# Optimization experiments

Measured on AMD Instinct MI355X. Metric: run time of the kernel, lower is better.

## Reference

```python
import jax, jax.numpy as jnp
import numpy as np

NUM_ITER = 3
HEADS = 8
EPS = 1e-8

def _ln(x, g, b, eps=1e-5):
    mu = x.mean(-1, keepdims=True)
    var = ((x - mu) ** 2).mean(-1, keepdims=True)
    return (x - mu) * jax.lax.rsqrt(var + eps) * g + b

def setup_inputs() -> dict:
    key = jax.random.key(0)
    ks = jax.random.split(key, 10)
    B, Nkv, Din = 32, 4096, 256
    Nq, S, Hm = 16, 256, 512
    def xav(k, shape):
        lim = (6.0 / (shape[0] + shape[1])) ** 0.5
        return jax.random.uniform(k, shape, minval=-lim, maxval=lim, dtype=jnp.float32)
    return {
        "slots": jax.random.normal(ks[0], (Nq, S), dtype=jnp.float32),
        "inputs": jax.random.normal(ks[1], (B, Nkv, Din), dtype=jnp.float32),
        "norm_in_g": jnp.ones((Din,), jnp.float32), "norm_in_b": jnp.zeros((Din,), jnp.float32),
        "norm_slots_g": jnp.ones((S,), jnp.float32), "norm_slots_b": jnp.zeros((S,), jnp.float32),
        "norm_mlp_g": jnp.ones((S,), jnp.float32), "norm_mlp_b": jnp.zeros((S,), jnp.float32),
        "Wq": xav(ks[2], (S, S)), "Wk": xav(ks[3], (S, Din)), "Wv": xav(ks[4], (S, Din)),
        "gru_wih": xav(ks[5], (3 * S, S)),
        "gru_whh": jax.random.normal(ks[6], (3 * S, S), dtype=jnp.float32) * (1.0 / S ** 0.5),
        "gru_bih": jnp.zeros((3 * S,), jnp.float32), "gru_bhh": jnp.zeros((3 * S,), jnp.float32),
        "mlp_w1": xav(ks[7], (Hm, S)), "mlp_b1": jnp.zeros((Hm,), jnp.float32),
        "mlp_w2": xav(ks[8], (S, Hm)), "mlp_b2": jnp.zeros((S,), jnp.float32),
    }

def reference(slots, inputs, norm_in_g, norm_in_b, norm_slots_g, norm_slots_b,
              norm_mlp_g, norm_mlp_b, Wq, Wk, Wv, gru_wih, gru_whh, gru_bih, gru_bhh,
              mlp_w1, mlp_b1, mlp_w2, mlp_b2):
    B, Nkv, Din = inputs.shape
    Nq, S = slots.shape
    H = HEADS
    hd = S // H
    slots = jnp.broadcast_to(slots, (B, Nq, S))
    x = _ln(inputs, norm_in_g, norm_in_b)
    k = (x @ Wk.T).reshape(B, Nkv, H, hd).transpose(0, 2, 1, 3) * (hd ** -0.5)  # [B,H,Nkv,hd]
    v = (x @ Wv.T).reshape(B, Nkv, H, hd).transpose(0, 2, 1, 3)
    attn_vis = None
    for _ in range(NUM_ITER):
        slots_prev = slots
        s = _ln(slots, norm_slots_g, norm_slots_b)
        q = (s @ Wq.T).reshape(B, Nq, H, hd).transpose(0, 2, 1, 3)  # [B,H,Nq,hd]
        # logits [B,Nkv,H*Nq]; softmax jointly over heads and slots per key (slot-axis softmax)
        logits = jnp.einsum('bhkd,bhqd->bkhq', k, q).reshape(B, Nkv, H * Nq)
        attn = jax.nn.softmax(logits, axis=-1).reshape(B, Nkv, H, Nq).transpose(0, 2, 1, 3)  # [B,H,Nkv,Nq]
        attn_vis = attn.sum(1)  # [B,Nkv,Nq]
        attn_n = attn / (attn.sum(axis=2, keepdims=True) + EPS)  # normalize over keys
        updates = jnp.einsum('bhkq,bhkd->bqhd', attn_n, v).reshape(B, Nq, S)
        # GRUCell: gates order r,z,n
        xg = updates.reshape(-1, S)
        h = slots_prev.reshape(-1, S)
        gi = xg @ gru_wih.T + gru_bih
        gh = h @ gru_whh.T + gru_bhh
        ir, iz, inn = jnp.split(gi, 3, axis=-1)
        hr, hz, hn = jnp.split(gh, 3, axis=-1)
        r = jax.nn.sigmoid(ir + hr)
        z = jax.nn.sigmoid(iz + hz)
        n = jnp.tanh(inn + r * hn)
        slots = ((1.0 - z) * n + z * h).reshape(B, Nq, S)
        m = _ln(slots, norm_mlp_g, norm_mlp_b)
        slots = slots + (jax.nn.relu(m @ mlp_w1.T + mlp_b1) @ mlp_w2.T + mlp_b2)
    return (slots, attn_vis)
```

## Files before the change

kernel.cpp:

```cpp
#include <hip/hip_runtime.h>
#include <stdint.h>

typedef unsigned short u16;
typedef __attribute__((ext_vector_type(8))) _Float16 half8;
typedef __attribute__((ext_vector_type(4))) _Float16 half4;
typedef __attribute__((ext_vector_type(4))) float floatx4;

__device__ inline float bflo(unsigned u){ return __uint_as_float(u << 16); }
__device__ inline float bfhi(unsigned u){ return __uint_as_float(u & 0xffff0000u); }
__device__ inline float bf1(u16 v){ return __uint_as_float(((unsigned)v) << 16); }
__device__ inline u16 f2bf(float f){
  unsigned u = __float_as_uint(f);
  u += 0x7fffu + ((u >> 16) & 1u);
  return (u16)(u >> 16);
}
__device__ inline float dot8(uint4 w, float4 a, float4 b, float acc){
  acc = fmaf(bflo(w.x), a.x, acc); acc = fmaf(bfhi(w.x), a.y, acc);
  acc = fmaf(bflo(w.y), a.z, acc); acc = fmaf(bfhi(w.y), a.w, acc);
  acc = fmaf(bflo(w.z), b.x, acc); acc = fmaf(bfhi(w.z), b.y, acc);
  acc = fmaf(bflo(w.w), b.z, acc); acc = fmaf(bfhi(w.w), b.w, acc);
  return acc;
}

#define CW_SLOTS 0
#define CW_GIN   4096
#define CW_BIN   4352
#define CW_GS    4608
#define CW_BS    4864
#define CW_GM    5120
#define CW_BM    5376
#define CW_WQ    5632
#define CW_WK    71168
#define CW_WV    136704
#define CW_WIH   202240
#define CW_WHH   398848
#define CW_BIH   595456
#define CW_BHH   596224
#define CW_W1    596992
#define CW_B1    728064
#define CW_W2    728576
#define CW_B2    859648
#define CW_TOTAL 859904

__global__ void k_flag(const u16* __restrict__ probe, int* __restrict__ flag){
  int t = threadIdx.x;
  int bad = 0;
  #pragma unroll
  for (int i = 0; i < 4; i++){
    float x = bf1(probe[t + i * 256]);
    if (!(fabsf(x) < 1e6f)) bad = 1;
  }
  __shared__ int s;
  if (t == 0) s = 0;
  __syncthreads();
  if (bad) atomicOr(&s, 1);
  __syncthreads();
  if (t == 0) *flag = s;
}

struct CanonArgs { const void* p[18]; };

__global__ void k_canon(CanonArgs a, const int* __restrict__ flag, u16* __restrict__ cw){
  const int off[19] = {CW_SLOTS, CW_GIN, CW_BIN, CW_GS, CW_BS, CW_GM, CW_BM, CW_WQ,
                       CW_WK, CW_WV, CW_WIH, CW_WHH, CW_BIH, CW_BHH, CW_W1, CW_B1,
                       CW_W2, CW_B2, CW_TOTAL};
  int i = blockIdx.x * 256 + threadIdx.x;
  if (i >= CW_TOTAL) return;
  int f32m = *flag;
  int j = 0;
  while (i >= off[j + 1]) j++;
  int local = i - off[j];
  float v = f32m ? ((const float*)a.p[j])[local] : bf1(((const u16*)a.p[j])[local]);
  cw[i] = f2bf(v);
}

__global__ void k_init(const u16* __restrict__ cw, float* __restrict__ slots,
                       _Float16* __restrict__ wkvh)
{
  int idx = blockIdx.x * 256 + threadIdx.x;
  if (idx < 131072){
    float g = bf1(cw[CW_GIN + (idx & 255)]);
    wkvh[idx] = (_Float16)(bf1(cw[CW_WK + idx]) * g);
  } else {
    int i = idx - 131072;
    int d = i & 255;
    int q = (i >> 8) & 15;
    slots[i] = bf1(cw[CW_SLOTS + q * 256 + d]);
  }
}

__global__ void k_beta(const u16* __restrict__ cw, float* __restrict__ beta){
  int c = blockIdx.x * 256 + threadIdx.x;
  if (c >= 512) return;
  float a = 0.f;
  for (int d = 0; d < 256; d++)
    a = fmaf(bf1(cw[CW_BIN + d]), bf1(cw[CW_WK + c * 256 + d]), a);
  beta[c] = a;
}

__global__ void k_zero(float* __restrict__ p, int n){
  int i = blockIdx.x * 256 + threadIdx.x;
  if (i < n) p[i] = 0.f;
}

__global__ __launch_bounds__(256) void k0_stats(
    const void* __restrict__ inp, const int* __restrict__ flag, float2* __restrict__ stats)
{
  int f32m = *flag;
  int g = blockIdx.x * 256 + threadIdx.x;
  int row = g >> 4, l = g & 15;
  float sum = 0.f, sq = 0.f;
  if (f32m){
    const float* rp = (const float*)inp + row * 256 + l * 16;
    #pragma unroll
    for (int i = 0; i < 4; i++){
      float4 v = ((const float4*)rp)[i];
      sum += v.x + v.y + v.z + v.w;
      sq = fmaf(v.x, v.x, sq); sq = fmaf(v.y, v.y, sq);
      sq = fmaf(v.z, v.z, sq); sq = fmaf(v.w, v.w, sq);
    }
  } else {
    const u16* rp = (const u16*)inp + row * 256 + l * 16;
    #pragma unroll
    for (int i = 0; i < 2; i++){
      uint4 u = ((const uint4*)rp)[i];
      unsigned w[4] = {u.x, u.y, u.z, u.w};
      #pragma unroll
      for (int p = 0; p < 4; p++){
        float a = bflo(w[p]), b = bfhi(w[p]);
        sum += a + b; sq = fmaf(a, a, sq); sq = fmaf(b, b, sq);
      }
    }
  }
  #pragma unroll
  for (int m = 1; m < 16; m <<= 1){ sum += __shfl_xor(sum, m); sq += __shfl_xor(sq, m); }
  if (l == 0){
    float mu = sum * (1.f/256.f);
    float var = sq * (1.f/256.f) - mu * mu;
    stats[row] = make_float2(mu, rsqrtf(var + 1e-5f));
  }
}

__global__ __launch_bounds__(256) void k1_gemm(
    const void* __restrict__ inp, const int* __restrict__ flag,
    const float2* __restrict__ stats, const float* __restrict__ beta,
    const _Float16* __restrict__ wkvh, _Float16* __restrict__ kh, _Float16* __restrict__ vT)
{
  int f32m = *flag;
  int tid = threadIdx.x;
  int wv = tid >> 6, lane = tid & 63;
  int m16 = lane & 15, q4 = lane >> 4;
  int nb = blockIdx.y;
  long rowb0 = (long)blockIdx.x * 128;
  int colW = nb * 256 + wv * 64;

  half8 bfr[4][8];
  #pragma unroll
  for (int nt = 0; nt < 4; nt++)
    #pragma unroll
    for (int s = 0; s < 8; s++)
      bfr[nt][s] = *(const half8*)(wkvh + (colW + nt * 16 + m16) * 256 + s * 32 + q4 * 8);

  float bet[4];
  #pragma unroll
  for (int nt = 0; nt < 4; nt++) bet[nt] = beta[colW + nt * 16 + m16];

  for (int rt = 0; rt < 8; rt++){
    long rowb = rowb0 + rt * 16;
    long myRow = rowb + m16;
    float2 st = stats[myRow];
    float mu = st.x, rstd = st.y;

    half8 af[8];
    if (f32m){
      const float* rp = (const float*)inp + myRow * 256 + q4 * 8;
      #pragma unroll
      for (int s = 0; s < 8; s++){
        float4 x0 = *(const float4*)(rp + s * 32);
        float4 x1 = *(const float4*)(rp + s * 32 + 4);
        af[s][0] = (_Float16)((x0.x - mu) * rstd); af[s][1] = (_Float16)((x0.y - mu) * rstd);
        af[s][2] = (_Float16)((x0.z - mu) * rstd); af[s][3] = (_Float16)((x0.w - mu) * rstd);
        af[s][4] = (_Float16)((x1.x - mu) * rstd); af[s][5] = (_Float16)((x1.y - mu) * rstd);
        af[s][6] = (_Float16)((x1.z - mu) * rstd); af[s][7] = (_Float16)((x1.w - mu) * rstd);
      }
    } else {
      const u16* rp = (const u16*)inp + myRow * 256 + q4 * 8;
      #pragma unroll
      for (int s = 0; s < 8; s++){
        uint4 xu = *(const uint4*)(rp + s * 32);
        unsigned xw[4] = {xu.x, xu.y, xu.z, xu.w};
        #pragma unroll
        for (int p = 0; p < 4; p++){
          af[s][2*p]   = (_Float16)((bflo(xw[p]) - mu) * rstd);
          af[s][2*p+1] = (_Float16)((bfhi(xw[p]) - mu) * rstd);
        }
      }
    }

    floatx4 acc[4];
    #pragma unroll
    for (int nt = 0; nt < 4; nt++){
      acc[nt][0] = bet[nt]; acc[nt][1] = bet[nt]; acc[nt][2] = bet[nt]; acc[nt][3] = bet[nt];
    }
    #pragma unroll
    for (int s = 0; s < 8; s++)
      #pragma unroll
      for (int nt = 0; nt < 4; nt++)
        acc[nt] = __builtin_amdgcn_mfma_f32_16x16x32_f16(af[s], bfr[nt][s], acc[nt], 0, 0, 0);

    if (nb == 0){
      long crow = rowb + q4 * 4;
      #pragma unroll
      for (int nt = 0; nt < 4; nt++)
        #pragma unroll
        for (int r = 0; r < 4; r++)
          kh[(crow + r) * 256 + colW + nt * 16 + m16] = (_Float16)acc[nt][r];
    } else {
      int b = (int)(rowb >> 12);
      int key = ((int)rowb & 4095) + q4 * 4;
      #pragma unroll
      for (int nt = 0; nt < 4; nt++){
        int cv = (colW - 256) + nt * 16 + m16;
        half4 pk;
        pk[0] = (_Float16)acc[nt][0]; pk[1] = (_Float16)acc[nt][1];
        pk[2] = (_Float16)acc[nt][2]; pk[3] = (_Float16)acc[nt][3];
        *(half4*)(vT + ((long)b * 256 + cv) * 4096 + key) = pk;
      }
    }
  }
}

__global__ __launch_bounds__(256) void k2_q(
    const float* __restrict__ slots, const u16* __restrict__ cw, _Float16* __restrict__ qh)
{
  const u16* gq = cw + CW_GS;
  const u16* bq = cw + CW_BS;
  const u16* Wq = cw + CW_WQ;
  int row = blockIdx.x, tid = threadIdx.x;
  int wv = tid >> 6, lane = tid & 63;
  float x = slots[row * 256 + tid];
  float s = x, s2 = x * x;
  #pragma unroll
  for (int m = 1; m < 64; m <<= 1){ s += __shfl_xor(s, m); s2 += __shfl_xor(s2, m); }
  __shared__ float red[8];
  if (lane == 0){ red[wv] = s; red[4 + wv] = s2; }
  __syncthreads();
  float tot  = red[0] + red[1] + red[2] + red[3];
  float tot2 = red[4] + red[5] + red[6] + red[7];
  float mu = tot * (1.f/256.f);
  float rstd = rsqrtf(tot2 * (1.f/256.f) - mu * mu + 1e-5f);
  __shared__ float sln[256];
  sln[tid] = (x - mu) * rstd * bf1(gq[tid]) + bf1(bq[tid]);
  __syncthreads();
  const u16* wr = Wq + tid * 256;
  float a = 0.f;
  for (int k = 0; k < 256; k += 8){
    uint4 wu = *(const uint4*)(wr + k);
    float4 l0 = *(const float4*)(sln + k);
    float4 l1 = *(const float4*)(sln + k + 4);
    a = dot8(wu, l0, l1, a);
  }
  qh[row * 256 + tid] = (_Float16)(a * 0.17677669529663687f);
}

__global__ __launch_bounds__(256) void k3_attn(
    const _Float16* __restrict__ kh, const _Float16* __restrict__ vT,
    const _Float16* __restrict__ qh,
    float* __restrict__ denom, float* __restrict__ numer,
    void* __restrict__ out_scratch, const int* __restrict__ flag, int lastIter)
{
  int f32m = *flag;
  int tid = threadIdx.x;
  int wv = tid >> 6, lane = tid & 63;
  int m16 = lane & 15, q4 = lane >> 4;
  int b = blockIdx.x, chunk = blockIdx.y;
  __shared__ float lds_l[32 * 129];

  half8 qf[2];
  #pragma unroll
  for (int hh = 0; hh < 2; hh++){
    int h = wv * 2 + hh;
    qf[hh] = *(const half8*)(qh + (b * 16 + m16) * 256 + h * 32 + q4 * 8);
  }
  float pd[2] = {0.f, 0.f};
  floatx4 un[2][2];
  #pragma unroll
  for (int hh = 0; hh < 2; hh++)
    #pragma unroll
    for (int dt = 0; dt < 2; dt++) un[hh][dt] = (floatx4)0.f;

  half8 afp[2][2];
  {
    int key0 = chunk * 256;
    #pragma unroll
    for (int sub = 0; sub < 2; sub++){
      long rowb = (long)b * 4096 + key0 + sub * 16;
      #pragma unroll
      for (int hh = 0; hh < 2; hh++)
        afp[sub][hh] = *(const half8*)(kh + (rowb + m16) * 256 + (wv * 2 + hh) * 32 + q4 * 8);
    }
  }

  floatx4 z4 = (floatx4)0.f;
  for (int g4 = 0; g4 < 8; g4++){
    int key0 = chunk * 256 + g4 * 32;
    #pragma unroll
    for (int sub = 0; sub < 2; sub++){
      #pragma unroll
      for (int hh = 0; hh < 2; hh++){
        int h = wv * 2 + hh;
        floatx4 d = __builtin_amdgcn_mfma_f32_16x16x32_f16(afp[sub][hh], qf[hh], z4, 0, 0, 0);
        #pragma unroll
        for (int r = 0; r < 4; r++)
          lds_l[(sub * 16 + q4 * 4 + r) * 129 + h * 16 + m16] = d[r];
      }
    }
    if (g4 < 7){
      int keyn = key0 + 32;
      #pragma unroll
      for (int sub = 0; sub < 2; sub++){
        long rowb = (long)b * 4096 + keyn + sub * 16;
        #pragma unroll
        for (int hh = 0; hh < 2; hh++)
          afp[sub][hh] = *(const half8*)(kh + (rowb + m16) * 256 + (wv * 2 + hh) * 32 + q4 * 8);
      }
    }
    __syncthreads();
    half8 vfr[2][2];
    #pragma unroll
    for (int hh = 0; hh < 2; hh++)
      #pragma unroll
      for (int dt = 0; dt < 2; dt++)
        vfr[hh][dt] = *(const half8*)(vT + ((long)b * 256 + (wv * 2 + hh) * 32 + dt * 16 + m16) * 4096 + key0 + q4 * 8);
    {
      int qq = tid & 15;
      #pragma unroll
      for (int half_ = 0; half_ < 2; half_++){
        int kk = (tid >> 4) + half_ * 16;
        float l[8];
        #pragma unroll
        for (int h8 = 0; h8 < 8; h8++) l[h8] = lds_l[kk * 129 + h8 * 16 + qq];
        float M = l[0];
        #pragma unroll
        for (int h8 = 1; h8 < 8; h8++) M = fmaxf(M, l[h8]);
        #pragma unroll
        for (int msk = 1; msk < 16; msk <<= 1) M = fmaxf(M, __shfl_xor(M, msk));
        float p[8], sl = 0.f;
        #pragma unroll
        for (int h8 = 0; h8 < 8; h8++){ p[h8] = __expf(l[h8] - M); sl += p[h8]; }
        float St = sl;
        #pragma unroll
        for (int msk = 1; msk < 16; msk <<= 1) St += __shfl_xor(St, msk);
        float rS = 1.f / St;
        if (lastIter){
          float av = sl * rS;
          long idx = 131072 + ((long)b * 4096 + key0 + kk) * 16 + qq;
          if (f32m) ((float*)out_scratch)[idx] = av;
          else      ((u16*)out_scratch)[idx]   = f2bf(av);
        }
        #pragma unroll
        for (int h8 = 0; h8 < 8; h8++) lds_l[kk * 129 + h8 * 16 + qq] = p[h8] * rS;
      }
    }
    __syncthreads();
    #pragma unroll
    for (int hh = 0; hh < 2; hh++){
      int h = wv * 2 + hh;
      float pv[8];
      #pragma unroll
      for (int j = 0; j < 8; j++) pv[j] = lds_l[(q4 * 8 + j) * 129 + h * 16 + m16];
      float ps = 0.f;
      #pragma unroll
      for (int j = 0; j < 8; j++) ps += pv[j];
      pd[hh] += ps;
      half8 bfr;
      #pragma unroll
      for (int j = 0; j < 8; j++) bfr[j] = (_Float16)pv[j];
      #pragma unroll
      for (int dt = 0; dt < 2; dt++)
        un[hh][dt] = __builtin_amdgcn_mfma_f32_16x16x32_f16(vfr[hh][dt], bfr, un[hh][dt], 0, 0, 0);
    }
    __syncthreads();
  }
  _Float16* pp = (_Float16*)((u16*)out_scratch + (f32m ? 262144 : 131072))
                 + (long)chunk * 131072;
  #pragma unroll
  for (int hh = 0; hh < 2; hh++){
    int h = wv * 2 + hh;
    float t = pd[hh];
    t += __shfl_xor(t, 16); t += __shfl_xor(t, 32);
    if (q4 == 0) atomicAdd(&denom[(b * 8 + h) * 16 + m16], t);
    if (lastIter){
      #pragma unroll
      for (int dt = 0; dt < 2; dt++)
        #pragma unroll
        for (int r = 0; r < 4; r++)
          atomicAdd(&numer[((b * 8 + h) * 16 + m16) * 32 + dt * 16 + q4 * 4 + r], un[hh][dt][r]);
    } else {
      #pragma unroll
      for (int dt = 0; dt < 2; dt++){
        half4 st;
        #pragma unroll
        for (int r = 0; r < 4; r++) st[r] = (_Float16)un[hh][dt][r];
        *(half4*)(pp + ((b * 8 + h) * 16 + m16) * 32 + dt * 16 + q4 * 4) = st;
      }
    }
  }
}

__global__ void k_reduce(const void* __restrict__ out_scratch, const int* __restrict__ flag,
                         float* __restrict__ numer){
  int i = blockIdx.x * 256 + threadIdx.x;
  int f32m = *flag;
  const _Float16* pp = (const _Float16*)((const u16*)out_scratch + (f32m ? 262144 : 131072));
  float s = 0.f;
  #pragma unroll
  for (int c = 0; c < 16; c++) s += (float)pp[(long)c * 131072 + i];
  numer[i] = s;
}

__global__ __launch_bounds__(256) void k4a_gru(
    const float* __restrict__ slots, const float* __restrict__ numer, const float* __restrict__ denom,
    const u16* __restrict__ cw, float* __restrict__ mid)
{
  const u16* wih = cw + CW_WIH;
  const u16* whh = cw + CW_WHH;
  const u16* bih = cw + CW_BIH;
  const u16* bhh = cw + CW_BHH;
  int jc = blockIdx.x, rg = blockIdx.y;
  int tid = threadIdx.x;
  __shared__ float u_s[8][256];
  __shared__ float h_s[8][256];
  {
    int hh = tid >> 5, dh = tid & 31;
    for (int i = 0; i < 8; i++){
      int row = rg * 8 + i;
      int b = row >> 4, slot = row & 15;
      float den = denom[(b * 8 + hh) * 16 + slot] + 1e-8f;
      u_s[i][tid] = numer[((b * 8 + hh) * 16 + slot) * 32 + dh] / den;
      h_s[i][tid] = slots[row * 256 + tid];
    }
  }
  __syncthreads();
  int rl = tid >> 5, jl = tid & 31;
  int j = jc * 32 + jl;
  int row = rg * 8 + rl;
  const u16* wir = wih + j * 256;
  const u16* wiz = wih + (256 + j) * 256;
  const u16* win = wih + (512 + j) * 256;
  const u16* whr = whh + j * 256;
  const u16* whz = whh + (256 + j) * 256;
  const u16* whn = whh + (512 + j) * 256;
  float air = 0, aiz = 0, ain = 0, ahr = 0, ahz = 0, ahn = 0;
  for (int k = 0; k < 256; k += 8){
    float4 u0 = *(const float4*)(&u_s[rl][k]);
    float4 u1 = *(const float4*)(&u_s[rl][k + 4]);
    float4 h0 = *(const float4*)(&h_s[rl][k]);
    float4 h1 = *(const float4*)(&h_s[rl][k + 4]);
    air = dot8(*(const uint4*)(wir + k), u0, u1, air);
    aiz = dot8(*(const uint4*)(wiz + k), u0, u1, aiz);
    ain = dot8(*(const uint4*)(win + k), u0, u1, ain);
    ahr = dot8(*(const uint4*)(whr + k), h0, h1, ahr);
    ahz = dot8(*(const uint4*)(whz + k), h0, h1, ahz);
    ahn = dot8(*(const uint4*)(whn + k), h0, h1, ahn);
  }
  float gr = air + bf1(bih[j])       + ahr + bf1(bhh[j]);
  float gz = aiz + bf1(bih[256 + j]) + ahz + bf1(bhh[256 + j]);
  float r = 1.f / (1.f + __expf(-gr));
  float z = 1.f / (1.f + __expf(-gz));
  float nn = tanhf(ain + bf1(bih[512 + j]) + r * (ahn + bf1(bhh[512 + j])));
  float h = h_s[rl][j];
  mid[row * 256 + j] = (1.f - z) * nn + z * h;
}

__global__ __launch_bounds__(256) void k4b_mlp(
    const float* __restrict__ mid, const u16* __restrict__ cw,
    float* __restrict__ slots, void* __restrict__ out_base,
    const int* __restrict__ flag, int lastIter)
{
  int f32m = *flag;
  const u16* gm = cw + CW_GM;
  const u16* bm = cw + CW_BM;
  const u16* w1 = cw + CW_W1;
  const u16* b1 = cw + CW_B1;
  const u16* w2 = cw + CW_W2;
  const u16* b2 = cw + CW_B2;
  int row = blockIdx.x, tid = threadIdx.x;
  int wv = tid >> 6, lane = tid & 63;
  float x = mid[row * 256 + tid];
  float s = x, s2 = x * x;
  #pragma unroll
  for (int m = 1; m < 64; m <<= 1){ s += __shfl_xor(s, m); s2 += __shfl_xor(s2, m); }
  __shared__ float red[8];
  if (lane == 0){ red[wv] = s; red[4 + wv] = s2; }
  __syncthreads();
  float tot  = red[0] + red[1] + red[2] + red[3];
  float tot2 = red[4] + red[5] + red[6] + red[7];
  float mu = tot * (1.f/256.f);
  float rstd = rsqrtf(tot2 * (1.f/256.f) - mu * mu + 1e-5f);
  __shared__ float ls[256];
  __shared__ float h1[512];
  ls[tid] = (x - mu) * rstd * bf1(gm[tid]) + bf1(bm[tid]);
  __syncthreads();
  const u16* w1a = w1 + tid * 256;
  const u16* w1b = w1 + (tid + 256) * 256;
  float a0 = 0.f, a1 = 0.f;
  for (int k = 0; k < 256; k += 8){
    float4 l0 = *(const float4*)(ls + k);
    float4 l1 = *(const float4*)(ls + k + 4);
    a0 = dot8(*(const uint4*)(w1a + k), l0, l1, a0);
    a1 = dot8(*(const uint4*)(w1b + k), l0, l1, a1);
  }
  h1[tid]       = fmaxf(a0 + bf1(b1[tid]), 0.f);
  h1[tid + 256] = fmaxf(a1 + bf1(b1[tid + 256]), 0.f);
  __syncthreads();
  const u16* w2r = w2 + tid * 512;
  float a = 0.f;
  for (int k = 0; k < 512; k += 8){
    float4 l0 = *(const float4*)(h1 + k);
    float4 l1 = *(const float4*)(h1 + k + 4);
    a = dot8(*(const uint4*)(w2r + k), l0, l1, a);
  }
  float res = x + a + bf1(b2[tid]);
  slots[row * 256 + tid] = res;
  if (lastIter){
    int idx = row * 256 + tid;
    if (f32m) ((float*)out_base)[idx] = res;
    else      ((u16*)out_base)[idx]   = f2bf(res);
  }
}

extern "C" void kernel_launch(void* const* d_in, const int* in_sizes, int n_in,
                              void* d_out, int out_size, void* d_ws, size_t ws_size,
                              hipStream_t stream)
{
  char* ws = (char*)d_ws;
  int*  flagp    = (int*)ws;
  u16*  cw       = (u16*)(ws + 256);
  _Float16* qh   = (_Float16*)(ws + 1720064);
  _Float16* wkvh = (_Float16*)(ws + 1982208);
  float* slots   = (float*)(ws + 2244352);
  float* mid     = (float*)(ws + 2768640);
  float* numer   = (float*)(ws + 3292928);
  float* denom   = (float*)(ws + 3817216);
  _Float16* kh   = (_Float16*)(ws + 3833600);
  _Float16* vT   = (_Float16*)(ws + 70942464);
  float2* stats  = (float2*)(ws + 2768640);
  float*  beta   = (float*)(ws + 3817216);

  CanonArgs ca;
  ca.p[0]  = d_in[0];   ca.p[1]  = d_in[2];   ca.p[2]  = d_in[3];
  ca.p[3]  = d_in[4];   ca.p[4]  = d_in[5];   ca.p[5]  = d_in[6];
  ca.p[6]  = d_in[7];   ca.p[7]  = d_in[8];   ca.p[8]  = d_in[9];
  ca.p[9]  = d_in[10];  ca.p[10] = d_in[11];  ca.p[11] = d_in[12];
  ca.p[12] = d_in[13];  ca.p[13] = d_in[14];  ca.p[14] = d_in[15];
  ca.p[15] = d_in[16];  ca.p[16] = d_in[17];  ca.p[17] = d_in[18];

  k_flag<<<1, 256, 0, stream>>>((const u16*)d_in[1], flagp);
  k_canon<<<(CW_TOTAL + 255) / 256, 256, 0, stream>>>(ca, flagp, cw);
  k_init<<<1024, 256, 0, stream>>>(cw, slots, wkvh);
  k_beta<<<2, 256, 0, stream>>>(cw, beta);
  k0_stats<<<8192, 256, 0, stream>>>(d_in[1], flagp, stats);
  k1_gemm<<<dim3(1024, 2), 256, 0, stream>>>(d_in[1], flagp, stats, beta, wkvh, kh, vT);
  for (int it = 0; it < 3; it++){
    int last = (it == 2) ? 1 : 0;
    k2_q<<<512, 256, 0, stream>>>(slots, cw, qh);
    if (last) k_zero<<<528, 256, 0, stream>>>(numer, 135168);
    else      k_zero<<<16, 256, 0, stream>>>(denom, 4096);
    k3_attn<<<dim3(32, 16), 256, 0, stream>>>(kh, vT, qh, denom, numer, d_out, flagp, last);
    if (!last) k_reduce<<<512, 256, 0, stream>>>(d_out, flagp, numer);
    k4a_gru<<<dim3(8, 64), 256, 0, stream>>>(slots, numer, denom, cw, mid);
    k4b_mlp<<<512, 256, 0, stream>>>(mid, cw, slots, d_out, flagp, last);
  }
}
```

Measured before the change: 791.4 us.

## Restructure K/V projection GEMM into narrower tiles with software-pipelined input loads

The K/V projection kernel now gives each wave a single 16-column tile instead of four, on a grid of 8 column blocks by 1024 row blocks. The next row tile's input loads are issued before the current tile's MFMAs run, so global load latency overlaps compute. The fp32/bf16 branch becomes a template parameter. In exchange, each input row is read and normalized four times more often, since each block now covers 64 columns rather than 256.

```diff
diff --git a/kernel.cpp b/kernel.cpp
--- a/kernel.cpp
+++ b/kernel.cpp
@@ -141,93 +141,111 @@
   }
 }
 
+template<int F32>
+__device__ __forceinline__ void k1_body(
+    const void* __restrict__ inp, const float2* __restrict__ stats,
+    const float* __restrict__ beta, const _Float16* __restrict__ wkvh,
+    _Float16* __restrict__ kh, _Float16* __restrict__ vT,
+    int nb, long rowb0, int colW, int m16, int q4)
+{
+  half8 bfr[8];
+  #pragma unroll
+  for (int s = 0; s < 8; s++)
+    bfr[s] = *(const half8*)(wkvh + (colW + m16) * 256 + s * 32 + q4 * 8);
+  float bet = beta[colW + m16];
+
+  constexpr int NR = F32 ? 16 : 8;
+  uint4 raw[NR];
+  half8 af[8];
+  float2 stp;
+
+  auto ISSUE = [&](long rowb){
+    long myRow = rowb + m16;
+    stp = stats[myRow];
+    if (F32){
+      const uint4* rp = (const uint4*)((const float*)inp + myRow * 256 + q4 * 8);
+      #pragma unroll
+      for (int s = 0; s < 8; s++){ raw[2*s] = rp[s*8]; raw[2*s+1] = rp[s*8+1]; }
+    } else {
+      const uint4* rp = (const uint4*)((const u16*)inp + myRow * 256 + q4 * 8);
+      #pragma unroll
+      for (int s = 0; s < 8; s++) raw[s] = rp[s*4];
+    }
+  };
+
+  auto CONVERT = [&](){
+    float mu = stp.x, rstd = stp.y;
+    if (F32){
+      #pragma unroll
+      for (int s = 0; s < 8; s++){
+        float x[8] = { __uint_as_float(raw[2*s].x), __uint_as_float(raw[2*s].y),
+                       __uint_as_float(raw[2*s].z), __uint_as_float(raw[2*s].w),
+                       __uint_as_float(raw[2*s+1].x), __uint_as_float(raw[2*s+1].y),
+                       __uint_as_float(raw[2*s+1].z), __uint_as_float(raw[2*s+1].w) };
+        #pragma unroll
+        for (int p = 0; p < 8; p++)
+          af[s][p] = (_Float16)((x[p] - mu) * rstd);
+      }
+    } else {
+      #pragma unroll
+      for (int s = 0; s < 8; s++){
+        unsigned xw[4] = {raw[s].x, raw[s].y, raw[s].z, raw[s].w};
+        #pragma unroll
+        for (int p = 0; p < 4; p++){
+          af[s][2*p]   = (_Float16)((bflo(xw[p]) - mu) * rstd);
+          af[s][2*p+1] = (_Float16)((bfhi(xw[p]) - mu) * rstd);
+        }
+      }
+    }
+  };
+
+  auto COMPUTE = [&](long rowb){
+    floatx4 acc;
+    acc[0] = bet; acc[1] = bet; acc[2] = bet; acc[3] = bet;
+    #pragma unroll
+    for (int s = 0; s < 8; s++)
+      acc = __builtin_amdgcn_mfma_f32_16x16x32_f16(af[s], bfr[s], acc, 0, 0, 0);
+
+    if (nb < 4){
+      long crow = rowb + q4 * 4;
+      #pragma unroll
+      for (int r = 0; r < 4; r++)
+        kh[(crow + r) * 256 + colW + m16] = (_Float16)acc[r];
+    } else {
+      int b = (int)(rowb >> 12);
+      int key = ((int)rowb & 4095) + q4 * 4;
+      int cv = (colW - 256) + m16;
+      half4 pk;
+      pk[0] = (_Float16)acc[0]; pk[1] = (_Float16)acc[1];
+      pk[2] = (_Float16)acc[2]; pk[3] = (_Float16)acc[3];
+      *(half4*)(vT + ((long)b * 256 + cv) * 4096 + key) = pk;
+    }
+  };
+
+  ISSUE(rowb0);
+  CONVERT();
+  #pragma unroll 1
+  for (int rt = 0; rt < 8; rt++){
+    if (rt < 7) ISSUE(rowb0 + (rt + 1) * 16);
+    COMPUTE(rowb0 + rt * 16);
+    if (rt < 7) CONVERT();
+  }
+}
+
 __global__ __launch_bounds__(256) void k1_gemm(
     const void* __restrict__ inp, const int* __restrict__ flag,
     const float2* __restrict__ stats, const float* __restrict__ beta,
     const _Float16* __restrict__ wkvh, _Float16* __restrict__ kh, _Float16* __restrict__ vT)
 {
-  int f32m = *flag;
   int tid = threadIdx.x;
   int wv = tid >> 6, lane = tid & 63;
   int m16 = lane & 15, q4 = lane >> 4;
-  int nb = blockIdx.y;
-  long rowb0 = (long)blockIdx.x * 128;
-  int colW = nb * 256 + wv * 64;
-
-  half8 bfr[4][8];
-  #pragma unroll
-  for (int nt = 0; nt < 4; nt++)
-    #pragma unroll
-    for (int s = 0; s < 8; s++)
-      bfr[nt][s] = *(const half8*)(wkvh + (colW + nt * 16 + m16) * 256 + s * 32 + q4 * 8);
-
-  float bet[4];
-  #pragma unroll
-  for (int nt = 0; nt < 4; nt++) bet[nt] = beta[colW + nt * 16 + m16];
-
-  for (int rt = 0; rt < 8; rt++){
-    long rowb = rowb0 + rt * 16;
-    long myRow = rowb + m16;
-    float2 st = stats[myRow];
-    float mu = st.x, rstd = st.y;
-
-    half8 af[8];
-    if (f32m){
-      const float* rp = (const float*)inp + myRow * 256 + q4 * 8;
-      #pragma unroll
-      for (int s = 0; s < 8; s++){
-        float4 x0 = *(const float4*)(rp + s * 32);
-        float4 x1 = *(const float4*)(rp + s * 32 + 4);
-        af[s][0] = (_Float16)((x0.x - mu) * rstd); af[s][1] = (_Float16)((x0.y - mu) * rstd);
-        af[s][2] = (_Float16)((x0.z - mu) * rstd); af[s][3] = (_Float16)((x0.w - mu) * rstd);
-        af[s][4] = (_Float16)((x1.x - mu) * rstd); af[s][5] = (_Float16)((x1.y - mu) * rstd);
-        af[s][6] = (_Float16)((x1.z - mu) * rstd); af[s][7] = (_Float16)((x1.w - mu) * rstd);
-      }
-    } else {
-      const u16* rp = (const u16*)inp + myRow * 256 + q4 * 8;
-      #pragma unroll
-      for (int s = 0; s < 8; s++){
-        uint4 xu = *(const uint4*)(rp + s * 32);
-        unsigned xw[4] = {xu.x, xu.y, xu.z, xu.w};
-        #pragma unroll
-        for (int p = 0; p < 4; p++){
-          af[s][2*p]   = (_Float16)((bflo(xw[p]) - mu) * rstd);
-          af[s][2*p+1] = (_Float16)((bfhi(xw[p]) - mu) * rstd);
-        }
-      }
-    }
-
-    floatx4 acc[4];
-    #pragma unroll
-    for (int nt = 0; nt < 4; nt++){
-      acc[nt][0] = bet[nt]; acc[nt][1] = bet[nt]; acc[nt][2] = bet[nt]; acc[nt][3] = bet[nt];
-    }
-    #pragma unroll
-    for (int s = 0; s < 8; s++)
-      #pragma unroll
-      for (int nt = 0; nt < 4; nt++)
-        acc[nt] = __builtin_amdgcn_mfma_f32_16x16x32_f16(af[s], bfr[nt][s], acc[nt], 0, 0, 0);
-
-    if (nb == 0){
-      long crow = rowb + q4 * 4;
-      #pragma unroll
-      for (int nt = 0; nt < 4; nt++)
-        #pragma unroll
-        for (int r = 0; r < 4; r++)
-          kh[(crow + r) * 256 + colW + nt * 16 + m16] = (_Float16)acc[nt][r];
-    } else {
-      int b = (int)(rowb >> 12);
-      int key = ((int)rowb & 4095) + q4 * 4;
-      #pragma unroll
-      for (int nt = 0; nt < 4; nt++){
-        int cv = (colW - 256) + nt * 16 + m16;
-        half4 pk;
-        pk[0] = (_Float16)acc[nt][0]; pk[1] = (_Float16)acc[nt][1];
-        pk[2] = (_Float16)acc[nt][2]; pk[3] = (_Float16)acc[nt][3];
-        *(half4*)(vT + ((long)b * 256 + cv) * 4096 + key) = pk;
-      }
-    }
-  }
+  int nb = blockIdx.x;
+  long rowb0 = (long)blockIdx.y * 128;
+  int colW = nb * 64 + wv * 16;
+
+  if (*flag) k1_body<1>(inp, stats, beta, wkvh, kh, vT, nb, rowb0, colW, m16, q4);
+  else       k1_body<0>(inp, stats, beta, wkvh, kh, vT, nb, rowb0, colW, m16, q4);
 }
 
 __global__ __launch_bounds__(256) void k2_q(
@@ -561,7 +579,7 @@
   k_init<<<1024, 256, 0, stream>>>(cw, slots, wkvh);
   k_beta<<<2, 256, 0, stream>>>(cw, beta);
   k0_stats<<<8192, 256, 0, stream>>>(d_in[1], flagp, stats);
-  k1_gemm<<<dim3(1024, 2), 256, 0, stream>>>(d_in[1], flagp, stats, beta, wkvh, kh, vT);
+  k1_gemm<<<dim3(8, 1024), 256, 0, stream>>>(d_in[1], flagp, stats, beta, wkvh, kh, vT);
   for (int it = 0; it < 3; it++){
     int last = (it == 2) ? 1 : 0;
     k2_q<<<512, 256, 0, stream>>>(slots, cw, qh);
```

New measurement: 1.130 ms. 1.43x slower.

## Tile V into 64-key blocks, process 64 keys per attention step, fuse zeroing

Applied to the files above, without the earlier changes.

The V transpose is now stored in 64-key tiles (batch, key group, channel, key) instead of one full 4096-key row per channel, so each attention step reads one compact tile. The attention loop handles 64 keys per iteration instead of 32, which halves the barrier and softmax round-trips per chunk but doubles the logit LDS buffer and the K fragment registers. The separate zeroing kernels for numer and denom are folded into the q-projection kernel, removing a launch per iteration. The larger LDS and register footprint could reduce occupancy.

```diff
diff --git a/kernel.cpp b/kernel.cpp
--- a/kernel.cpp
+++ b/kernel.cpp
@@ -98,11 +98,6 @@
   beta[c] = a;
 }
 
-__global__ void k_zero(float* __restrict__ p, int n){
-  int i = blockIdx.x * 256 + threadIdx.x;
-  if (i < n) p[i] = 0.f;
-}
-
 __global__ __launch_bounds__(256) void k0_stats(
     const void* __restrict__ inp, const int* __restrict__ flag, float2* __restrict__ stats)
 {
@@ -218,25 +213,30 @@
     } else {
       int b = (int)(rowb >> 12);
       int key = ((int)rowb & 4095) + q4 * 4;
+      int kg  = key >> 6;
+      int klo = key & 63;
       #pragma unroll
       for (int nt = 0; nt < 4; nt++){
         int cv = (colW - 256) + nt * 16 + m16;
         half4 pk;
         pk[0] = (_Float16)acc[nt][0]; pk[1] = (_Float16)acc[nt][1];
         pk[2] = (_Float16)acc[nt][2]; pk[3] = (_Float16)acc[nt][3];
-        *(half4*)(vT + ((long)b * 256 + cv) * 4096 + key) = pk;
+        *(half4*)(vT + (((long)b * 64 + kg) * 256 + cv) * 64 + klo) = pk;
       }
     }
   }
 }
 
 __global__ __launch_bounds__(256) void k2_q(
-    const float* __restrict__ slots, const u16* __restrict__ cw, _Float16* __restrict__ qh)
+    const float* __restrict__ slots, const u16* __restrict__ cw, _Float16* __restrict__ qh,
+    float* __restrict__ denom, float* __restrict__ numer, int lastIter)
 {
   const u16* gq = cw + CW_GS;
   const u16* bq = cw + CW_BS;
   const u16* Wq = cw + CW_WQ;
   int row = blockIdx.x, tid = threadIdx.x;
+  if (lastIter) numer[row * 256 + tid] = 0.f;
+  if (row < 16) denom[row * 256 + tid] = 0.f;
   int wv = tid >> 6, lane = tid & 63;
   float x = slots[row * 256 + tid];
   float s = x, s2 = x * x;
@@ -274,7 +274,7 @@
   int wv = tid >> 6, lane = tid & 63;
   int m16 = lane & 15, q4 = lane >> 4;
   int b = blockIdx.x, chunk = blockIdx.y;
-  __shared__ float lds_l[32 * 129];
+  __shared__ float lds_l[64 * 129];
 
   half8 qf[2];
   #pragma unroll
@@ -289,11 +289,11 @@
     #pragma unroll
     for (int dt = 0; dt < 2; dt++) un[hh][dt] = (floatx4)0.f;
 
-  half8 afp[2][2];
+  half8 afp[4][2];
   {
     int key0 = chunk * 256;
     #pragma unroll
-    for (int sub = 0; sub < 2; sub++){
+    for (int sub = 0; sub < 4; sub++){
       long rowb = (long)b * 4096 + key0 + sub * 16;
       #pragma unroll
       for (int hh = 0; hh < 2; hh++)
@@ -302,10 +302,10 @@
   }
 
   floatx4 z4 = (floatx4)0.f;
-  for (int g4 = 0; g4 < 8; g4++){
-    int key0 = chunk * 256 + g4 * 32;
-    #pragma unroll
-    for (int sub = 0; sub < 2; sub++){
+  for (int grp = 0; grp < 4; grp++){
+    int key0 = chunk * 256 + grp * 64;
+    #pragma unroll
+    for (int sub = 0; sub < 4; sub++){
       #pragma unroll
       for (int hh = 0; hh < 2; hh++){
         int h = wv * 2 + hh;
@@ -315,10 +315,10 @@
           lds_l[(sub * 16 + q4 * 4 + r) * 129 + h * 16 + m16] = d[r];
       }
     }
-    if (g4 < 7){
-      int keyn = key0 + 32;
-      #pragma unroll
-      for (int sub = 0; sub < 2; sub++){
+    if (grp < 3){
+      int keyn = key0 + 64;
+      #pragma unroll
+      for (int sub = 0; sub < 4; sub++){
         long rowb = (long)b * 4096 + keyn + sub * 16;
         #pragma unroll
         for (int hh = 0; hh < 2; hh++)
@@ -326,16 +326,23 @@
       }
     }
     __syncthreads();
-    half8 vfr[2][2];
-    #pragma unroll
-    for (int hh = 0; hh < 2; hh++)
-      #pragma unroll
-      for (int dt = 0; dt < 2; dt++)
-        vfr[hh][dt] = *(const half8*)(vT + ((long)b * 256 + (wv * 2 + hh) * 32 + dt * 16 + m16) * 4096 + key0 + q4 * 8);
+    half8 vfr[2][2][2];
+    {
+      int kg = key0 >> 6;
+      #pragma unroll
+      for (int ks = 0; ks < 2; ks++)
+        #pragma unroll
+        for (int hh = 0; hh < 2; hh++)
+          #pragma unroll
+          for (int dt = 0; dt < 2; dt++)
+            vfr[ks][hh][dt] = *(const half8*)(vT +
+                (((long)b * 64 + kg) * 256 + (wv * 2 + hh) * 32 + dt * 16 + m16) * 64
+                + ks * 32 + q4 * 8);
+    }
     {
       int qq = tid & 15;
       #pragma unroll
-      for (int half_ = 0; half_ < 2; half_++){
+      for (int half_ = 0; half_ < 4; half_++){
         int kk = (tid >> 4) + half_ * 16;
         float l[8];
         #pragma unroll
@@ -366,19 +373,22 @@
     #pragma unroll
     for (int hh = 0; hh < 2; hh++){
       int h = wv * 2 + hh;
-      float pv[8];
-      #pragma unroll
-      for (int j = 0; j < 8; j++) pv[j] = lds_l[(q4 * 8 + j) * 129 + h * 16 + m16];
-      float ps = 0.f;
-      #pragma unroll
-      for (int j = 0; j < 8; j++) ps += pv[j];
-      pd[hh] += ps;
-      half8 bfr;
-      #pragma unroll
-      for (int j = 0; j < 8; j++) bfr[j] = (_Float16)pv[j];
-      #pragma unroll
-      for (int dt = 0; dt < 2; dt++)
-        un[hh][dt] = __builtin_amdgcn_mfma_f32_16x16x32_f16(vfr[hh][dt], bfr, un[hh][dt], 0, 0, 0);
+      #pragma unroll
+      for (int ks = 0; ks < 2; ks++){
+        float pv[8];
+        #pragma unroll
+        for (int j = 0; j < 8; j++) pv[j] = lds_l[(ks * 32 + q4 * 8 + j) * 129 + h * 16 + m16];
+        float ps = 0.f;
+        #pragma unroll
+        for (int j = 0; j < 8; j++) ps += pv[j];
+        pd[hh] += ps;
+        half8 bfr;
+        #pragma unroll
+        for (int j = 0; j < 8; j++) bfr[j] = (_Float16)pv[j];
+        #pragma unroll
+        for (int dt = 0; dt < 2; dt++)
+          un[hh][dt] = __builtin_amdgcn_mfma_f32_16x16x32_f16(vfr[ks][hh][dt], bfr, un[hh][dt], 0, 0, 0);
+      }
     }
     __syncthreads();
   }
@@ -564,9 +574,7 @@
   k1_gemm<<<dim3(1024, 2), 256, 0, stream>>>(d_in[1], flagp, stats, beta, wkvh, kh, vT);
   for (int it = 0; it < 3; it++){
     int last = (it == 2) ? 1 : 0;
-    k2_q<<<512, 256, 0, stream>>>(slots, cw, qh);
-    if (last) k_zero<<<528, 256, 0, stream>>>(numer, 135168);
-    else      k_zero<<<16, 256, 0, stream>>>(denom, 4096);
+    k2_q<<<512, 256, 0, stream>>>(slots, cw, qh, denom, numer, last);
     k3_attn<<<dim3(32, 16), 256, 0, stream>>>(kh, vT, qh, denom, numer, d_out, flagp, last);
     if (!last) k_reduce<<<512, 256, 0, stream>>>(d_out, flagp, numer);
     k4a_gru<<<dim3(8, 64), 256, 0, stream>>>(slots, numer, denom, cw, mid);
```

Result: no change. 789.2 us (-0.3%).
